# Optimization experiments

Hardware: AMD Instinct MI355X
Metric: run time of the kernel (lower is better)

Reference implementation:

```python
import jax, jax.numpy as jnp
import numpy as np

N = 2048      # number of ROIs
C = 1024      # in_channels == inter_channels
G = 16        # groups
D = C // G    # per-group dim = 64


def _bbox_overlaps(b1, b2):
    # mmdet-1.x IoU with +1 pixel convention; b1:(N,4), b2:(M,4)
    area1 = (b1[:, 2] - b1[:, 0] + 1) * (b1[:, 3] - b1[:, 1] + 1)  # (N,)
    area2 = (b2[:, 2] - b2[:, 0] + 1) * (b2[:, 3] - b2[:, 1] + 1)  # (M,)
    lt = jnp.maximum(b1[:, None, :2], b2[None, :, :2])             # (N,M,2)
    rb = jnp.minimum(b1[:, None, 2:], b2[None, :, 2:])             # (N,M,2)
    wh = jnp.clip(rb - lt + 1, 0)
    inter = wh[..., 0] * wh[..., 1]                                # (N,M)
    return inter / (area1[:, None] + area2[None, :] - inter)


def setup_inputs() -> dict:
    key = jax.random.key(0)
    ks = jax.random.split(key, 9)
    in_x = jax.random.normal(ks[0], (N, C), dtype=jnp.float32)
    # valid boxes: [batch_idx, x1, y1, x2, y2]
    xy = jax.random.uniform(ks[1], (N, 2), minval=0.0, maxval=800.0)
    wh = jax.random.uniform(ks[2], (N, 2), minval=8.0, maxval=200.0)
    rois = jnp.concatenate([jnp.zeros((N, 1)), xy, xy + wh], axis=1).astype(jnp.float32)
    s = 1.0 / np.sqrt(C)
    W0 = jax.random.normal(ks[3], (C, C), dtype=jnp.float32) * s
    b0 = jnp.zeros((C,), dtype=jnp.float32)
    W1 = jax.random.normal(ks[4], (C, C), dtype=jnp.float32) * s
    b1 = jnp.zeros((C,), dtype=jnp.float32)
    # grouped 1x1 conv: per group maps C channels -> D channels
    Wout = jax.random.normal(ks[5], (G, D, C), dtype=jnp.float32) * s
    bout = jnp.zeros((C,), dtype=jnp.float32)
    return {"in_x": in_x, "rois": rois, "W0": W0, "b0": b0, "W1": W1,
            "b1": b1, "Wout": Wout, "bout": bout}


def reference(in_x, rois, W0, b0, W1, b1, Wout, bout):
    # self-attention path: in_ref_x = in_x, ref_rois = rois
    # embed convs are pre-activation (relu -> 1x1 conv), shared for x and ref_x
    def embed(v):
        v = jax.nn.relu(v) @ W0.T + b0
        v = jax.nn.relu(v) @ W1.T + b1
        return v
    x = embed(in_x)                      # (N, C)
    ref_x = x                            # shared convs, same input
    xg = x.reshape(N, G, D)
    rg = ref_x.reshape(N, G, D)
    scores = jnp.einsum('ngd,mgd->ngm', xg, rg) / jnp.sqrt(jnp.float32(D))  # (N,G,N)
    ious = _bbox_overlaps(rois[:, 1:], rois[:, 1:])                          # (N,N)
    scores = scores + jnp.log(ious[:, None, :] + 1e-6)
    attn = jax.nn.softmax(scores, axis=2)                                    # (N,G,N)
    y = jnp.einsum('ngm,mc->ngc', attn, in_x)                                # (N,G,C)
    out = jnp.einsum('ngc,goc->ngo', y, Wout).reshape(N, C) + bout           # (N,C)
    return out
```

## Files before the change

### kernel.cpp

```cpp
#include <hip/hip_runtime.h>
#include <math.h>

constexpr int NROI = 2048;
constexpr int CDIM = 1024;
constexpr int NG   = 16;
constexpr int DH   = 64;

typedef __attribute__((ext_vector_type(8))) short short8;
typedef __attribute__((ext_vector_type(4))) float floatx4;

#define MFMA_BF16(a, b, c) __builtin_amdgcn_mfma_f32_16x16x32_bf16((a), (b), (c), 0, 0, 0)

__device__ __forceinline__ short f2bf(float f) {
  unsigned u = __float_as_uint(f);
  unsigned r = 0x7fffu + ((u >> 16) & 1u);
  return (short)((u + r) >> 16);
}
__device__ __forceinline__ float bf2f(unsigned short u) {
  return __uint_as_float(((unsigned)u) << 16);
}
__device__ __forceinline__ unsigned pack2(float a, float b) {
  return (unsigned)(unsigned short)f2bf(a) | ((unsigned)(unsigned short)f2bf(b) << 16);
}

__device__ __forceinline__ unsigned cvtpk_bf16(float lo, float hi) {
  unsigned r;
  asm("v_cvt_pk_bf16_f32 %0, %1, %2" : "=v"(r) : "v"(lo), "v"(hi));
  return r;
}

__device__ __forceinline__ float fexp2(float x) {
#if __has_builtin(__builtin_amdgcn_exp2f)
  return __builtin_amdgcn_exp2f(x);
#else
  return __expf(x * 0.69314718056f);
#endif
}

typedef __attribute__((address_space(1))) void GV;
typedef __attribute__((address_space(3))) void LV;
__device__ __forceinline__ void gl2lds16(const void* g, void* l) {
  __builtin_amdgcn_global_load_lds((GV*)g, (LV*)l, 16, 0, 0);
}

__device__ __forceinline__ short8 brelu(short8 v) {
  union { short8 s; unsigned u[4]; } x; x.s = v;
#pragma unroll
  for (int i = 0; i < 4; ++i) {
    unsigned m = (x.u[i] >> 15) & 0x10001u;
    x.u[i] &= ~(m * 0xFFFFu);
  }
  return x.s;
}

__device__ __forceinline__ int keypos(int k) {
  return (k & ~31) | (((k >> 2) & 3) << 3) | (((k >> 4) & 1) << 2);
}

__global__ __launch_bounds__(512) void prep_kernel(
    const float* __restrict__ in_x, const float* __restrict__ W0,
    const float* __restrict__ W1, const float* __restrict__ Wout,
    const float* __restrict__ rois,
    short* __restrict__ xin_b, short* __restrict__ W0b,
    short* __restrict__ W1b, short* __restrict__ Woutb,
    unsigned short* __restrict__ biasb)
{
  const int gi = blockIdx.x * 512 + threadIdx.x;
  if (gi < 524288) {
    const float4 v = ((const float4*)in_x)[gi];
    uint2 u; u.x = pack2(v.x, v.y); u.y = pack2(v.z, v.w);
    ((uint2*)xin_b)[gi] = u;
  }
  if (gi < 262144) {
    float4 v = ((const float4*)W0)[gi];
    uint2 u; u.x = pack2(v.x, v.y); u.y = pack2(v.z, v.w);
    ((uint2*)W0b)[gi] = u;
    v = ((const float4*)W1)[gi];
    u.x = pack2(v.x, v.y); u.y = pack2(v.z, v.w);
    ((uint2*)W1b)[gi] = u;
    v = ((const float4*)Wout)[gi];
    u.x = pack2(v.x, v.y); u.y = pack2(v.z, v.w);
    ((uint2*)Woutb)[gi] = u;
  }
  const int q  = gi >> 9;
  const int k0 = (gi & 511) * 4;
  const float qx1 = rois[q * 5 + 1], qy1 = rois[q * 5 + 2];
  const float qx2 = rois[q * 5 + 3], qy2 = rois[q * 5 + 4];
  const float qa = (qx2 - qx1 + 1.f) * (qy2 - qy1 + 1.f);
  float v[4];
#pragma unroll
  for (int j = 0; j < 4; ++j) {
    const int k = k0 + j;
    const float kx1 = rois[k * 5 + 1], ky1 = rois[k * 5 + 2];
    const float kx2 = rois[k * 5 + 3], ky2 = rois[k * 5 + 4];
    const float ka = (kx2 - kx1 + 1.f) * (ky2 - ky1 + 1.f);
    float iw = fminf(qx2, kx2) - fmaxf(qx1, kx1) + 1.f;
    float ih = fminf(qy2, ky2) - fmaxf(qy1, ky1) + 1.f;
    iw = fmaxf(iw, 0.f); ih = fmaxf(ih, 0.f);
    const float inter = iw * ih;
    v[j] = inter * __builtin_amdgcn_rcpf(qa + ka - inter) + 1e-6f;
  }
  uint2 u; u.x = pack2(v[0], v[1]); u.y = pack2(v[2], v[3]);
  *(uint2*)&biasb[(size_t)q * NROI + keypos(k0)] = u;
}

template <int FUSED>
__global__ __launch_bounds__(256, 4) void gemm64(
    const short* __restrict__ A, const short* __restrict__ Ba,
    const short* __restrict__ Bb, const float* __restrict__ bias,
    short* __restrict__ outRM, short* __restrict__ outTR)
{
  __shared__ short As[2][8 * 512];
  __shared__ short Bs[2][8 * 512];
  const int t = threadIdx.x, w = t >> 6, lane = t & 63;
  const int wm = w >> 1, wn = w & 1;
  const int row0 = blockIdx.y * 64;
  bool isW0; int col0; const short* B;
  if (FUSED) {
    isW0 = blockIdx.x < 16;
    col0 = (blockIdx.x & 15) * 64;
    B = isW0 ? Ba : Bb;
  } else {
    isW0 = true; col0 = blockIdx.x * 64; B = Ba;
  }
  const bool doRelu = FUSED ? isW0 : true;
  const int rlo = lane & 15, khi = (lane >> 4) * 8;

  floatx4 acc[2][2];
#pragma unroll
  for (int i = 0; i < 2; ++i)
#pragma unroll
    for (int j = 0; j < 2; ++j) acc[i][j] = (floatx4){0.f, 0.f, 0.f, 0.f};

#pragma unroll
  for (int kh = 0; kh < 2; ++kh) {
    const int f = w * 2 + kh;
    gl2lds16(A + (size_t)(row0 + w * 16 + rlo) * CDIM + kh * 32 + khi, &As[0][f * 512]);
    gl2lds16(B + (size_t)(col0 + w * 16 + rlo) * CDIM + kh * 32 + khi, &Bs[0][f * 512]);
  }
  __syncthreads();

  for (int it = 0; it < 16; ++it) {
    const int p = it & 1;
    if (it < 15) {
      const int k1 = (it + 1) * 64;
#pragma unroll
      for (int kh = 0; kh < 2; ++kh) {
        const int f = w * 2 + kh;
        gl2lds16(A + (size_t)(row0 + w * 16 + rlo) * CDIM + k1 + kh * 32 + khi,
                 &As[1 - p][f * 512]);
        gl2lds16(B + (size_t)(col0 + w * 16 + rlo) * CDIM + k1 + kh * 32 + khi,
                 &Bs[1 - p][f * 512]);
      }
    }
#pragma unroll
    for (int kh = 0; kh < 2; ++kh) {
      short8 a[2], bf[2];
#pragma unroll
      for (int i = 0; i < 2; ++i) {
        a[i] = *(const short8*)&As[p][((wm * 2 + i) * 2 + kh) * 512 + lane * 8];
        if (doRelu) a[i] = brelu(a[i]);
      }
#pragma unroll
      for (int j = 0; j < 2; ++j)
        bf[j] = *(const short8*)&Bs[p][((wn * 2 + j) * 2 + kh) * 512 + lane * 8];
#pragma unroll
      for (int i = 0; i < 2; ++i)
#pragma unroll
        for (int j = 0; j < 2; ++j)
          acc[i][j] = MFMA_BF16(a[i], bf[j], acc[i][j]);
    }
    __syncthreads();
  }

  const int colL = lane & 15, qq = lane >> 4;
  if (!FUSED || isW0) {
    float bj[2];
    bj[0] = bias[col0 + wn * 32 + colL];
    bj[1] = bias[col0 + wn * 32 + 16 + colL];
#pragma unroll
    for (int i = 0; i < 2; ++i)
#pragma unroll
      for (int j = 0; j < 2; ++j)
#pragma unroll
        for (int r = 0; r < 4; ++r) {
          const int row = row0 + wm * 32 + i * 16 + qq * 4 + r;
          const int cc  = col0 + wn * 32 + j * 16 + colL;
          outRM[(size_t)row * CDIM + cc] = f2bf(acc[i][j][r] + bj[j]);
        }
  } else {
#pragma unroll
    for (int i = 0; i < 2; ++i)
#pragma unroll
      for (int j = 0; j < 2; ++j) {
        unsigned long long u =
            (unsigned long long)pack2(acc[i][j][0], acc[i][j][1]) |
            ((unsigned long long)pack2(acc[i][j][2], acc[i][j][3]) << 32);
        const int cc  = col0 + wn * 32 + j * 16 + colL;
        const int row = row0 + wm * 32 + i * 16 + qq * 4;
        *(unsigned long long*)&outTR[(size_t)cc * NROI + keypos(row)] = u;
      }
  }
}

__global__ __launch_bounds__(1024) void attn_bias(
    const short* __restrict__ Xb,
    const short* __restrict__ ZTb,
    const unsigned short* __restrict__ biasb,
    const float* __restrict__ bout,
    float* __restrict__ Out)
{
  const int lin  = blockIdx.x + 16 * blockIdx.y;
  const int xcd  = lin & 7;
  const int slot = lin >> 3;
  const int g    = 2 * xcd + (slot >> 4);
  const int n0   = (slot & 15) * 128;

  const int t    = threadIdx.x;
  const int w    = t >> 6;
  const int qt   = w >> 2;
  const int wq   = w & 3;
  const int lane = t & 63;
  const int col  = lane & 15;
  const int qq   = lane >> 4;
  const int rlo  = col, khi = qq * 8;

  __shared__ short Kq[4][2][4096];
  __shared__ short Vq[4][2][4096];

  short8 qf[2][2];
#pragma unroll
  for (int s = 0; s < 2; ++s) {
    const size_t qoff = (size_t)(n0 + wq * 32 + s * 16 + col) * CDIM + g * DH;
    qf[s][0] = *(const short8*)(Xb + qoff + qq * 8);
    qf[s][1] = *(const short8*)(Xb + qoff + 32 + qq * 8);
  }

  short8 ONES;
#pragma unroll
  for (int i = 0; i < 8; ++i) ONES[i] = (short)0x3F80;

  floatx4 oc[2][4];
#pragma unroll
  for (int s = 0; s < 2; ++s)
#pragma unroll
    for (int dt = 0; dt < 4; ++dt) oc[s][dt] = (floatx4){0.f, 0.f, 0.f, 0.f};
  floatx4 lsA[2];
  lsA[0] = (floatx4){0.f, 0.f, 0.f, 0.f};
  lsA[1] = (floatx4){0.f, 0.f, 0.f, 0.f};

  const int kb = qt * 512;

#pragma unroll
  for (int kh = 0; kh < 2; ++kh) {
    gl2lds16(Xb + (size_t)(kb + wq * 16 + rlo) * CDIM + g * DH + kh * 32 + khi,
             &Kq[qt][0][(wq * 2 + kh) * 512]);
    gl2lds16(ZTb + (size_t)(g * DH + wq * 16 + rlo) * NROI + kb + kh * 32 + khi,
             &Vq[qt][0][(wq * 2 + kh) * 512]);
  }
  __syncthreads();

  const unsigned short* bq0 =
      biasb + (size_t)(n0 + wq * 32 + col) * NROI + kb + qq * 8;
  const unsigned short* bq1 = bq0 + (size_t)16 * NROI;

  for (int it = 0; it < 8; ++it) {
    const int p  = it & 1;
    const int m0 = kb + it * 64;

    union { short8 s8[4]; unsigned short h[32]; } BU;
    BU.s8[0] = *(const short8*)(bq0 + it * 64);
    BU.s8[1] = *(const short8*)(bq0 + it * 64 + 32);
    BU.s8[2] = *(const short8*)(bq1 + it * 64);
    BU.s8[3] = *(const short8*)(bq1 + it * 64 + 32);

    if (it + 1 < 8) {
      const int m1 = m0 + 64;
#pragma unroll
      for (int kh = 0; kh < 2; ++kh) {
        gl2lds16(Xb + (size_t)(m1 + wq * 16 + rlo) * CDIM + g * DH + kh * 32 + khi,
                 &Kq[qt][1 - p][(wq * 2 + kh) * 512]);
        gl2lds16(ZTb + (size_t)(g * DH + wq * 16 + rlo) * NROI + m1 + kh * 32 + khi,
                 &Vq[qt][1 - p][(wq * 2 + kh) * 512]);
      }
    }

    union { short8 s; unsigned u[4]; } U[2][2];
#pragma unroll
    for (int ct = 0; ct < 4; ++ct) {
      const short8 k0 = *(const short8*)&Kq[qt][p][(ct * 2 + 0) * 512 + lane * 8];
      const short8 k1 = *(const short8*)&Kq[qt][p][(ct * 2 + 1) * 512 + lane * 8];
#pragma unroll
      for (int s = 0; s < 2; ++s) {
        floatx4 z4 = (floatx4){0.f, 0.f, 0.f, 0.f};
        z4 = MFMA_BF16(k0, qf[s][0], z4);
        z4 = MFMA_BF16(k1, qf[s][1], z4);
        float pv0 = fexp2(z4[0] * 0.18033688011f) * bf2f(BU.h[s * 16 + ct * 4 + 0]);
        float pv1 = fexp2(z4[1] * 0.18033688011f) * bf2f(BU.h[s * 16 + ct * 4 + 1]);
        float pv2 = fexp2(z4[2] * 0.18033688011f) * bf2f(BU.h[s * 16 + ct * 4 + 2]);
        float pv3 = fexp2(z4[3] * 0.18033688011f) * bf2f(BU.h[s * 16 + ct * 4 + 3]);
        U[s][ct >> 1].u[(ct & 1) * 2 + 0] = cvtpk_bf16(pv0, pv1);
        U[s][ct >> 1].u[(ct & 1) * 2 + 1] = cvtpk_bf16(pv2, pv3);
      }
    }

    lsA[0] = MFMA_BF16(U[0][0].s, ONES, lsA[0]);
    lsA[0] = MFMA_BF16(U[0][1].s, ONES, lsA[0]);
    lsA[1] = MFMA_BF16(U[1][0].s, ONES, lsA[1]);
    lsA[1] = MFMA_BF16(U[1][1].s, ONES, lsA[1]);

#pragma unroll
    for (int dt = 0; dt < 4; ++dt) {
      const short8 v0 = *(const short8*)&Vq[qt][p][(dt * 2 + 0) * 512 + lane * 8];
      const short8 v1 = *(const short8*)&Vq[qt][p][(dt * 2 + 1) * 512 + lane * 8];
#pragma unroll
      for (int s = 0; s < 2; ++s) {
        oc[s][dt] = MFMA_BF16(U[s][0].s, v0, oc[s][dt]);
        oc[s][dt] = MFMA_BF16(U[s][1].s, v1, oc[s][dt]);
      }
    }
    __syncthreads();
  }

  float* kbuf = (float*)&Kq[0][0][0];
  float* vbuf = (float*)&Vq[0][0][0];
  const int wslot = (qt - 1) * 4 + wq;
  if (qt != 0) {
#pragma unroll
    for (int dt = 0; dt < 4; ++dt)
#pragma unroll
      for (int r = 0; r < 4; ++r) {
        kbuf[(dt * 4 + r) * 768 + wslot * 64 + lane] = oc[0][dt][r];
        vbuf[(dt * 4 + r) * 768 + wslot * 64 + lane] = oc[1][dt][r];
      }
    if (col == 0) {
#pragma unroll
      for (int s = 0; s < 2; ++s)
#pragma unroll
        for (int r = 0; r < 4; ++r)
          kbuf[12288 + wslot * 32 + s * 16 + qq * 4 + r] = lsA[s][r];
    }
  }
  __syncthreads();
  if (qt == 0) {
    float ls[2][4];
#pragma unroll
    for (int s = 0; s < 2; ++s)
#pragma unroll
      for (int r = 0; r < 4; ++r) ls[s][r] = lsA[s][r];
#pragma unroll
    for (int j = 0; j < 3; ++j) {
      const int ws = j * 4 + wq;
#pragma unroll
      for (int dt = 0; dt < 4; ++dt)
#pragma unroll
        for (int r = 0; r < 4; ++r) {
          oc[0][dt][r] += kbuf[(dt * 4 + r) * 768 + ws * 64 + lane];
          oc[1][dt][r] += vbuf[(dt * 4 + r) * 768 + ws * 64 + lane];
        }
#pragma unroll
      for (int s = 0; s < 2; ++s)
#pragma unroll
        for (int r = 0; r < 4; ++r)
          ls[s][r] += kbuf[12288 + ws * 32 + s * 16 + qq * 4 + r];
    }
#pragma unroll
    for (int s = 0; s < 2; ++s) {
      float rinv[4];
#pragma unroll
      for (int r = 0; r < 4; ++r)
        rinv[r] = __builtin_amdgcn_rcpf(ls[s][r]);
#pragma unroll
      for (int dt = 0; dt < 4; ++dt) {
        const float bo = bout[g * DH + dt * 16 + col];
#pragma unroll
        for (int r = 0; r < 4; ++r)
          Out[(size_t)(n0 + wq * 32 + s * 16 + qq * 4 + r) * CDIM + g * DH +
              dt * 16 + col] = oc[s][dt][r] * rinv[r] + bo;
      }
    }
  }
}

extern "C" void kernel_launch(void* const* d_in, const int* in_sizes, int n_in,
                              void* d_out, int out_size, void* d_ws, size_t ws_size,
                              hipStream_t stream) {
  const float* in_x = (const float*)d_in[0];
  const float* rois = (const float*)d_in[1];
  const float* W0   = (const float*)d_in[2];
  const float* b0   = (const float*)d_in[3];
  const float* W1   = (const float*)d_in[4];
  const float* b1   = (const float*)d_in[5];
  const float* Wout = (const float*)d_in[6];
  const float* bout = (const float*)d_in[7];
  char* w8 = (char*)d_ws;

  short* xin_b = (short*)w8;
  short* W0b   = (short*)(w8 + ((size_t)4 << 20));
  short* W1b   = (short*)(w8 + ((size_t)6 << 20));
  short* Woutb = (short*)(w8 + ((size_t)8 << 20));
  short* zT    = (short*)(w8 + ((size_t)10 << 20));
  unsigned short* biasb = (unsigned short*)(w8 + ((size_t)14 << 20));
  short* xb  = xin_b;
  short* t0b = (short*)d_out;

  prep_kernel<<<2048, 512, 0, stream>>>(in_x, W0, W1, Wout, rois,
                                        xin_b, W0b, W1b, Woutb, biasb);
  gemm64<1><<<dim3(32, 32), 256, 0, stream>>>(xin_b, W0b, Woutb, b0, t0b, zT);
  gemm64<0><<<dim3(16, 32), 256, 0, stream>>>(t0b, W1b, nullptr, b1, xb, nullptr);
  attn_bias<<<dim3(16, 16), 1024, 0, stream>>>(xb, zT, biasb, bout,
                                               (float*)d_out);
}
```

Measured before the change: 179.2 us.

## Fuse fp32-to-bf16 conversion and IoU bias into GEMM kernels, drop prep kernel

Removes the separate prep kernel. The embedding GEMMs now read fp32 inputs and weights directly, convert them to bf16 in registers and store them to LDS. The IoU log-bias table is computed at the tail of the first GEMM kernel. This saves a launch and the write-then-read of the bf16 copies. In exchange the GEMMs fetch twice the bytes per operand, repeat the conversion in every tile, and stage loads through registers instead of asynchronous global-to-LDS transfers, which may reduce overlap.

```diff
diff --git a/kernel.cpp b/kernel.cpp
--- a/kernel.cpp
+++ b/kernel.cpp
@@ -27,6 +27,15 @@
   unsigned r;
   asm("v_cvt_pk_bf16_f32 %0, %1, %2" : "=v"(r) : "v"(lo), "v"(hi));
   return r;
+}
+
+__device__ __forceinline__ short8 cvt8(float4 v0, float4 v1) {
+  union { short8 s; unsigned u[4]; } r;
+  r.u[0] = cvtpk_bf16(v0.x, v0.y);
+  r.u[1] = cvtpk_bf16(v0.z, v0.w);
+  r.u[2] = cvtpk_bf16(v1.x, v1.y);
+  r.u[3] = cvtpk_bf16(v1.z, v1.w);
+  return r.s;
 }
 
 __device__ __forceinline__ float fexp2(float x) {
@@ -57,74 +66,24 @@
   return (k & ~31) | (((k >> 2) & 3) << 3) | (((k >> 4) & 1) << 2);
 }
 
-__global__ __launch_bounds__(512) void prep_kernel(
-    const float* __restrict__ in_x, const float* __restrict__ W0,
-    const float* __restrict__ W1, const float* __restrict__ Wout,
-    const float* __restrict__ rois,
-    short* __restrict__ xin_b, short* __restrict__ W0b,
-    short* __restrict__ W1b, short* __restrict__ Woutb,
+__global__ __launch_bounds__(256, 4) void gemm1f(
+    const float* __restrict__ Xf, const float* __restrict__ W0f,
+    const float* __restrict__ Woutf, const float* __restrict__ rois,
+    const float* __restrict__ bias,
+    short* __restrict__ outRM, short* __restrict__ outTR,
     unsigned short* __restrict__ biasb)
-{
-  const int gi = blockIdx.x * 512 + threadIdx.x;
-  if (gi < 524288) {
-    const float4 v = ((const float4*)in_x)[gi];
-    uint2 u; u.x = pack2(v.x, v.y); u.y = pack2(v.z, v.w);
-    ((uint2*)xin_b)[gi] = u;
-  }
-  if (gi < 262144) {
-    float4 v = ((const float4*)W0)[gi];
-    uint2 u; u.x = pack2(v.x, v.y); u.y = pack2(v.z, v.w);
-    ((uint2*)W0b)[gi] = u;
-    v = ((const float4*)W1)[gi];
-    u.x = pack2(v.x, v.y); u.y = pack2(v.z, v.w);
-    ((uint2*)W1b)[gi] = u;
-    v = ((const float4*)Wout)[gi];
-    u.x = pack2(v.x, v.y); u.y = pack2(v.z, v.w);
-    ((uint2*)Woutb)[gi] = u;
-  }
-  const int q  = gi >> 9;
-  const int k0 = (gi & 511) * 4;
-  const float qx1 = rois[q * 5 + 1], qy1 = rois[q * 5 + 2];
-  const float qx2 = rois[q * 5 + 3], qy2 = rois[q * 5 + 4];
-  const float qa = (qx2 - qx1 + 1.f) * (qy2 - qy1 + 1.f);
-  float v[4];
-#pragma unroll
-  for (int j = 0; j < 4; ++j) {
-    const int k = k0 + j;
-    const float kx1 = rois[k * 5 + 1], ky1 = rois[k * 5 + 2];
-    const float kx2 = rois[k * 5 + 3], ky2 = rois[k * 5 + 4];
-    const float ka = (kx2 - kx1 + 1.f) * (ky2 - ky1 + 1.f);
-    float iw = fminf(qx2, kx2) - fmaxf(qx1, kx1) + 1.f;
-    float ih = fminf(qy2, ky2) - fmaxf(qy1, ky1) + 1.f;
-    iw = fmaxf(iw, 0.f); ih = fmaxf(ih, 0.f);
-    const float inter = iw * ih;
-    v[j] = inter * __builtin_amdgcn_rcpf(qa + ka - inter) + 1e-6f;
-  }
-  uint2 u; u.x = pack2(v[0], v[1]); u.y = pack2(v[2], v[3]);
-  *(uint2*)&biasb[(size_t)q * NROI + keypos(k0)] = u;
-}
-
-template <int FUSED>
-__global__ __launch_bounds__(256, 4) void gemm64(
-    const short* __restrict__ A, const short* __restrict__ Ba,
-    const short* __restrict__ Bb, const float* __restrict__ bias,
-    short* __restrict__ outRM, short* __restrict__ outTR)
 {
   __shared__ short As[2][8 * 512];
   __shared__ short Bs[2][8 * 512];
   const int t = threadIdx.x, w = t >> 6, lane = t & 63;
   const int wm = w >> 1, wn = w & 1;
   const int row0 = blockIdx.y * 64;
-  bool isW0; int col0; const short* B;
-  if (FUSED) {
-    isW0 = blockIdx.x < 16;
-    col0 = (blockIdx.x & 15) * 64;
-    B = isW0 ? Ba : Bb;
-  } else {
-    isW0 = true; col0 = blockIdx.x * 64; B = Ba;
-  }
-  const bool doRelu = FUSED ? isW0 : true;
+  const bool isW0 = blockIdx.x < 16;
+  const int col0 = (blockIdx.x & 15) * 64;
+  const float* Bf = isW0 ? W0f : Woutf;
   const int rlo = lane & 15, khi = (lane >> 4) * 8;
+  const int arow = row0 + w * 16 + rlo;
+  const int brow = col0 + w * 16 + rlo;
 
   floatx4 acc[2][2];
 #pragma unroll
@@ -134,23 +93,26 @@
 
 #pragma unroll
   for (int kh = 0; kh < 2; ++kh) {
-    const int f = w * 2 + kh;
-    gl2lds16(A + (size_t)(row0 + w * 16 + rlo) * CDIM + kh * 32 + khi, &As[0][f * 512]);
-    gl2lds16(B + (size_t)(col0 + w * 16 + rlo) * CDIM + kh * 32 + khi, &Bs[0][f * 512]);
+    const float* pa = Xf + (size_t)arow * CDIM + kh * 32 + khi;
+    const float* pb = Bf + (size_t)brow * CDIM + kh * 32 + khi;
+    *(short8*)&As[0][(w * 2 + kh) * 512 + lane * 8] =
+        cvt8(*(const float4*)pa, *(const float4*)(pa + 4));
+    *(short8*)&Bs[0][(w * 2 + kh) * 512 + lane * 8] =
+        cvt8(*(const float4*)pb, *(const float4*)(pb + 4));
   }
   __syncthreads();
 
   for (int it = 0; it < 16; ++it) {
     const int p = it & 1;
+    float4 la[2][2], lb[2][2];
     if (it < 15) {
       const int k1 = (it + 1) * 64;
 #pragma unroll
       for (int kh = 0; kh < 2; ++kh) {
-        const int f = w * 2 + kh;
-        gl2lds16(A + (size_t)(row0 + w * 16 + rlo) * CDIM + k1 + kh * 32 + khi,
-                 &As[1 - p][f * 512]);
-        gl2lds16(B + (size_t)(col0 + w * 16 + rlo) * CDIM + k1 + kh * 32 + khi,
-                 &Bs[1 - p][f * 512]);
+        const float* pa = Xf + (size_t)arow * CDIM + k1 + kh * 32 + khi;
+        const float* pb = Bf + (size_t)brow * CDIM + k1 + kh * 32 + khi;
+        la[kh][0] = *(const float4*)pa;  la[kh][1] = *(const float4*)(pa + 4);
+        lb[kh][0] = *(const float4*)pb;  lb[kh][1] = *(const float4*)(pb + 4);
       }
     }
 #pragma unroll
@@ -159,7 +121,7 @@
 #pragma unroll
       for (int i = 0; i < 2; ++i) {
         a[i] = *(const short8*)&As[p][((wm * 2 + i) * 2 + kh) * 512 + lane * 8];
-        if (doRelu) a[i] = brelu(a[i]);
+        if (isW0) a[i] = brelu(a[i]);
       }
 #pragma unroll
       for (int j = 0; j < 2; ++j)
@@ -170,11 +132,18 @@
         for (int j = 0; j < 2; ++j)
           acc[i][j] = MFMA_BF16(a[i], bf[j], acc[i][j]);
     }
+    if (it < 15) {
+#pragma unroll
+      for (int kh = 0; kh < 2; ++kh) {
+        *(short8*)&As[1 - p][(w * 2 + kh) * 512 + lane * 8] = cvt8(la[kh][0], la[kh][1]);
+        *(short8*)&Bs[1 - p][(w * 2 + kh) * 512 + lane * 8] = cvt8(lb[kh][0], lb[kh][1]);
+      }
+    }
     __syncthreads();
   }
 
   const int colL = lane & 15, qq = lane >> 4;
-  if (!FUSED || isW0) {
+  if (isW0) {
     float bj[2];
     bj[0] = bias[col0 + wn * 32 + colL];
     bj[1] = bias[col0 + wn * 32 + 16 + colL];
@@ -201,6 +170,116 @@
         *(unsigned long long*)&outTR[(size_t)cc * NROI + keypos(row)] = u;
       }
   }
+
+  {
+    const int tid = (blockIdx.y * 32 + blockIdx.x) * 256 + threadIdx.x;
+    const int q   = tid >> 7;
+    const int k0  = (tid & 127) * 16;
+    const float qx1 = rois[q * 5 + 1], qy1 = rois[q * 5 + 2];
+    const float qx2 = rois[q * 5 + 3], qy2 = rois[q * 5 + 4];
+    const float qa = (qx2 - qx1 + 1.f) * (qy2 - qy1 + 1.f);
+#pragma unroll
+    for (int b = 0; b < 4; ++b) {
+      const int kk = k0 + b * 4;
+      float v[4];
+#pragma unroll
+      for (int j = 0; j < 4; ++j) {
+        const int k = kk + j;
+        const float kx1 = rois[k * 5 + 1], ky1 = rois[k * 5 + 2];
+        const float kx2 = rois[k * 5 + 3], ky2 = rois[k * 5 + 4];
+        const float ka = (kx2 - kx1 + 1.f) * (ky2 - ky1 + 1.f);
+        float iw = fminf(qx2, kx2) - fmaxf(qx1, kx1) + 1.f;
+        float ih = fminf(qy2, ky2) - fmaxf(qy1, ky1) + 1.f;
+        iw = fmaxf(iw, 0.f); ih = fmaxf(ih, 0.f);
+        const float inter = iw * ih;
+        v[j] = inter * __builtin_amdgcn_rcpf(qa + ka - inter) + 1e-6f;
+      }
+      uint2 u; u.x = pack2(v[0], v[1]); u.y = pack2(v[2], v[3]);
+      *(uint2*)&biasb[(size_t)q * NROI + keypos(kk)] = u;
+    }
+  }
+}
+
+__global__ __launch_bounds__(256, 4) void gemm2f(
+    const short* __restrict__ A, const float* __restrict__ W1f,
+    const float* __restrict__ bias, short* __restrict__ outRM)
+{
+  __shared__ short As[2][8 * 512];
+  __shared__ short Bs[2][8 * 512];
+  const int t = threadIdx.x, w = t >> 6, lane = t & 63;
+  const int wm = w >> 1, wn = w & 1;
+  const int row0 = blockIdx.y * 64;
+  const int col0 = blockIdx.x * 64;
+  const int rlo = lane & 15, khi = (lane >> 4) * 8;
+  const int brow = col0 + w * 16 + rlo;
+
+  floatx4 acc[2][2];
+#pragma unroll
+  for (int i = 0; i < 2; ++i)
+#pragma unroll
+    for (int j = 0; j < 2; ++j) acc[i][j] = (floatx4){0.f, 0.f, 0.f, 0.f};
+
+#pragma unroll
+  for (int kh = 0; kh < 2; ++kh) {
+    gl2lds16(A + (size_t)(row0 + w * 16 + rlo) * CDIM + kh * 32 + khi,
+             &As[0][(w * 2 + kh) * 512]);
+    const float* pb = W1f + (size_t)brow * CDIM + kh * 32 + khi;
+    *(short8*)&Bs[0][(w * 2 + kh) * 512 + lane * 8] =
+        cvt8(*(const float4*)pb, *(const float4*)(pb + 4));
+  }
+  __syncthreads();
+
+  for (int it = 0; it < 16; ++it) {
+    const int p = it & 1;
+    float4 lb[2][2];
+    if (it < 15) {
+      const int k1 = (it + 1) * 64;
+#pragma unroll
+      for (int kh = 0; kh < 2; ++kh) {
+        gl2lds16(A + (size_t)(row0 + w * 16 + rlo) * CDIM + k1 + kh * 32 + khi,
+                 &As[1 - p][(w * 2 + kh) * 512]);
+        const float* pb = W1f + (size_t)brow * CDIM + k1 + kh * 32 + khi;
+        lb[kh][0] = *(const float4*)pb;  lb[kh][1] = *(const float4*)(pb + 4);
+      }
+    }
+#pragma unroll
+    for (int kh = 0; kh < 2; ++kh) {
+      short8 a[2], bf[2];
+#pragma unroll
+      for (int i = 0; i < 2; ++i) {
+        a[i] = brelu(*(const short8*)&As[p][((wm * 2 + i) * 2 + kh) * 512 + lane * 8]);
+      }
+#pragma unroll
+      for (int j = 0; j < 2; ++j)
+        bf[j] = *(const short8*)&Bs[p][((wn * 2 + j) * 2 + kh) * 512 + lane * 8];
+#pragma unroll
+      for (int i = 0; i < 2; ++i)
+#pragma unroll
+        for (int j = 0; j < 2; ++j)
+          acc[i][j] = MFMA_BF16(a[i], bf[j], acc[i][j]);
+    }
+    if (it < 15) {
+#pragma unroll
+      for (int kh = 0; kh < 2; ++kh)
+        *(short8*)&Bs[1 - p][(w * 2 + kh) * 512 + lane * 8] = cvt8(lb[kh][0], lb[kh][1]);
+    }
+    __syncthreads();
+  }
+
+  const int colL = lane & 15, qq = lane >> 4;
+  float bj[2];
+  bj[0] = bias[col0 + wn * 32 + colL];
+  bj[1] = bias[col0 + wn * 32 + 16 + colL];
+#pragma unroll
+  for (int i = 0; i < 2; ++i)
+#pragma unroll
+    for (int j = 0; j < 2; ++j)
+#pragma unroll
+      for (int r = 0; r < 4; ++r) {
+        const int row = row0 + wm * 32 + i * 16 + qq * 4 + r;
+        const int cc  = col0 + wn * 32 + j * 16 + colL;
+        outRM[(size_t)row * CDIM + cc] = f2bf(acc[i][j][r] + bj[j]);
+      }
 }
 
 __global__ __launch_bounds__(1024) void attn_bias(
@@ -395,19 +474,14 @@
   const float* bout = (const float*)d_in[7];
   char* w8 = (char*)d_ws;
 
-  short* xin_b = (short*)w8;
-  short* W0b   = (short*)(w8 + ((size_t)4 << 20));
-  short* W1b   = (short*)(w8 + ((size_t)6 << 20));
-  short* Woutb = (short*)(w8 + ((size_t)8 << 20));
+  short* xb    = (short*)w8;
   short* zT    = (short*)(w8 + ((size_t)10 << 20));
   unsigned short* biasb = (unsigned short*)(w8 + ((size_t)14 << 20));
-  short* xb  = xin_b;
   short* t0b = (short*)d_out;
 
-  prep_kernel<<<2048, 512, 0, stream>>>(in_x, W0, W1, Wout, rois,
-                                        xin_b, W0b, W1b, Woutb, biasb);
-  gemm64<1><<<dim3(32, 32), 256, 0, stream>>>(xin_b, W0b, Woutb, b0, t0b, zT);
-  gemm64<0><<<dim3(16, 32), 256, 0, stream>>>(t0b, W1b, nullptr, b1, xb, nullptr);
+  gemm1f<<<dim3(32, 32), 256, 0, stream>>>(in_x, W0, Wout, rois, b0,
+                                           t0b, zT, biasb);
+  gemm2f<<<dim3(16, 32), 256, 0, stream>>>(t0b, W1, b1, xb);
   attn_bias<<<dim3(16, 16), 1024, 0, stream>>>(xb, zT, biasb, bout,
                                                (float*)d_out);
 }
```

Result: slower. 207.3 us (+15.7%).
